# Performance work log

Measured on AMD Instinct MI355X. Metric: run time of the kernel, lower is better.

Reference implementation:

```python
import jax, jax.numpy as jnp
import numpy as np

B, S, E = 8, 4096, 2048
LATENT, HEAD = 64, 128


def setup_inputs() -> dict:
    key = jax.random.key(0)
    ks = jax.random.split(key, 5)
    sd = lambda n: 1.0 / np.sqrt(n)
    return {
        "x": jax.random.normal(ks[0], (B, S, E), dtype=jnp.float32),
        "w_dkv": jax.random.normal(ks[1], (E, LATENT), dtype=jnp.float32) * sd(E),
        "w_k": jax.random.normal(ks[2], (LATENT, HEAD), dtype=jnp.float32) * sd(LATENT),
        "w_v": jax.random.normal(ks[3], (LATENT, HEAD), dtype=jnp.float32) * sd(LATENT),
        "w_q": jax.random.normal(ks[4], (E, HEAD), dtype=jnp.float32) * sd(E),
    }


def reference(x, w_dkv, w_k, w_v, w_q):
    # x: [B,S,E]. kv_cache=None path: cache = fresh compressed latents.
    latent = jnp.einsum('bse,el->bsl', x, w_dkv)          # [B,S,latent] compressed KV cache
    k = jnp.einsum('bsl,lh->bsh', latent, w_k)            # decompress keys   [B,S,head]
    v = jnp.einsum('bsl,lh->bsh', latent, w_v)            # decompress values [B,S,head]
    q = jnp.einsum('bse,eh->bsh', x, w_q)                 # queries [B,S,head]
    scale = w_q.shape[-1] ** -0.5
    scores = jnp.einsum('bqh,bkh->bqk', q, k) * scale     # [B,S,S]
    seq = x.shape[1]
    causal = jnp.tril(jnp.ones((seq, seq), dtype=bool))   # tril(seq, cache_len)
    scores = jnp.where(causal, scores, -jnp.inf)
    attn = jax.nn.softmax(scores, axis=-1)                # dropout p=0 (eval)
    out = jnp.einsum('bqk,bkh->bqh', attn, v)             # [B,S,head]
    return out, latent
```

## Files before the change

### kernel.cpp

```cpp
#include <hip/hip_runtime.h>

typedef __bf16 bf16;
typedef __bf16 bf16x2 __attribute__((ext_vector_type(2)));
typedef __bf16 bf16x4 __attribute__((ext_vector_type(4)));
typedef __bf16 bf16x8 __attribute__((ext_vector_type(8)));
typedef float  f32x4  __attribute__((ext_vector_type(4)));

#define MFMA16(a,b,c) __builtin_amdgcn_mfma_f32_16x16x32_bf16((a),(b),(c),0,0,0)

constexpr int Bn = 8, Sn = 4096, En = 2048, Ln = 64, Hn = 128;
constexpr int Mrows = Bn * Sn;

__device__ __forceinline__ void load_lds_16(const bf16* g, bf16* l) {
    __builtin_amdgcn_global_load_lds(
        (const __attribute__((address_space(1))) uint32_t*)g,
        (__attribute__((address_space(3))) uint32_t*)l, 16, 0, 0);
}

__global__ __launch_bounds__(256) void transpose_cvt(const float* __restrict__ in,
                                                     bf16* __restrict__ out,
                                                     int K, int N) {
    int tid = blockIdx.x * 256 + threadIdx.x;
    if (tid >= K * N) return;
    int k = tid / N, n = tid - k * N;
    out[n * K + k] = (bf16)in[tid];
}

__global__ __launch_bounds__(512) void gemm_xw(const float* __restrict__ x,
                                               const bf16* __restrict__ wT,
                                               const bf16* __restrict__ wkT,
                                               const bf16* __restrict__ wvT,
                                               float* __restrict__ latent_out,
                                               bf16* __restrict__ q_out,
                                               bf16* __restrict__ k_out,
                                               bf16* __restrict__ vT_out) {
    __shared__ __align__(16) bf16 As[64 * 72];
    __shared__ __align__(16) bf16 Bs[192 * 64];
    const int lane = threadIdx.x & 63;
    const int wave = threadIdx.x >> 6;
    const int col  = lane & 15, quad = lane >> 4;
    const int mgrp  = wave >> 1;
    const int nhalf = wave & 1;
    const int mblock = blockIdx.x * 64;

    f32x4 acc[6];
#pragma unroll
    for (int t = 0; t < 6; ++t) acc[t] = (f32x4){0.f, 0.f, 0.f, 0.f};

    const int bsub = lane >> 3;
    const int bkg0 = lane & 7;
    const int akc  = threadIdx.x & 15;
    const int arow0 = threadIdx.x >> 4;

    for (int step = 0; step < 32; ++step) {
        __syncthreads();
#pragma unroll
        for (int j = 0; j < 3; ++j) {
            int nr0 = wave * 24 + j * 8;
            int n = nr0 + bsub;
            int kgrp = bkg0 ^ bsub;
            const bf16* g = wT + (size_t)n * En + step * 64 + kgrp * 8;
            load_lds_16(g, &Bs[nr0 * 64]);
        }
#pragma unroll
        for (int p = 0; p < 2; ++p) {
            int row = p * 32 + arow0;
            f32x4 v = *(const f32x4*)(x + (size_t)(mblock + row) * En + step * 64 + akc * 4);
            bf16x4 c;
#pragma unroll
            for (int j = 0; j < 4; ++j) c[j] = (bf16)v[j];
            *(bf16x4*)(&As[row * 72 + akc * 4]) = c;
        }
        __syncthreads();
#pragma unroll
        for (int ks2 = 0; ks2 < 2; ++ks2) {
            bf16x8 a = *(const bf16x8*)(&As[(mgrp * 16 + col) * 72 + ks2 * 32 + quad * 8]);
#pragma unroll
            for (int t = 0; t < 6; ++t) {
                int n = nhalf * 96 + t * 16 + col;
                int sg = (ks2 * 4 + quad) ^ (col & 7);
                bf16x8 b = *(const bf16x8*)(&Bs[n * 64 + sg * 8]);
                acc[t] = MFMA16(a, b, acc[t]);
            }
        }
    }
    __syncthreads();
    if (nhalf == 0) {
#pragma unroll
        for (int t = 0; t < 4; ++t)
#pragma unroll
            for (int r = 0; r < 4; ++r)
                As[(mgrp * 16 + quad * 4 + r) * 72 + t * 16 + col] = (bf16)acc[t][r];
    }
#pragma unroll
    for (int t = 0; t < 6; ++t) {
        int gnt = nhalf * 6 + t;
#pragma unroll
        for (int r = 0; r < 4; ++r) {
            int row = mblock + mgrp * 16 + quad * 4 + r;
            if (gnt < 4) latent_out[(size_t)row * Ln + gnt * 16 + col] = acc[t][r];
            else         q_out[(size_t)row * Hn + (gnt - 4) * 16 + col] = (bf16)acc[t][r];
        }
    }
    __syncthreads();
    const bf16* w2 = (nhalf == 0) ? wkT : wvT;
    f32x4 kv[8];
#pragma unroll
    for (int nt = 0; nt < 8; ++nt) kv[nt] = (f32x4){0.f, 0.f, 0.f, 0.f};
#pragma unroll
    for (int ks = 0; ks < 2; ++ks) {
        bf16x8 a = *(const bf16x8*)(&As[(mgrp * 16 + col) * 72 + ks * 32 + quad * 8]);
#pragma unroll
        for (int nt = 0; nt < 8; ++nt) {
            bf16x8 b = *(const bf16x8*)(w2 + (nt * 16 + col) * Ln + ks * 32 + quad * 8);
            kv[nt] = MFMA16(a, b, kv[nt]);
        }
    }
    if (nhalf == 0) {
#pragma unroll
        for (int nt = 0; nt < 8; ++nt)
#pragma unroll
            for (int r = 0; r < 4; ++r) {
                int row = mblock + mgrp * 16 + quad * 4 + r;
                k_out[(size_t)row * Hn + nt * 16 + col] = (bf16)kv[nt][r];
            }
    } else {
        int bb = mblock >> 12;
        int sbase = (mblock & 4095) + mgrp * 16 + quad * 4;
#pragma unroll
        for (int nt = 0; nt < 8; ++nt) {
            bf16x4 pv;
#pragma unroll
            for (int r = 0; r < 4; ++r) pv[r] = (bf16)kv[nt][r];
            *(bf16x4*)(vT_out + ((size_t)bb * Hn + nt * 16 + col) * Sn + sbase) = pv;
        }
    }
}

__global__ __launch_bounds__(256, 3) void mla_attn(const bf16* __restrict__ qg,
                                                   const bf16* __restrict__ kg,
                                                   const bf16* __restrict__ vtg,
                                                   float* __restrict__ outg) {
    __shared__ __align__(16) bf16 Ks[64 * 128];
    __shared__ __align__(16) bf16 VtS[128 * 64];
    __shared__ __align__(16) bf16 Pb[4][16][72];
    const int lane = threadIdx.x & 63;
    const int wave = threadIdx.x >> 6;
    const int col  = lane & 15, quad = lane >> 4;
    const int rank  = blockIdx.x;
    const int qtile = 63 - (rank >> 3);
    const int bb    = rank & 7;
    const int qbase = qtile * 64;
    const bf16* kb  = kg  + (size_t)bb * Sn * Hn;
    const bf16* vbT = vtg + (size_t)bb * Sn * Hn;

    bf16x8 qf[4];
    {
        const bf16* qrow = qg + ((size_t)bb * Sn + qbase + wave * 16 + col) * Hn;
#pragma unroll
        for (int ks = 0; ks < 4; ++ks)
            qf[ks] = *(const bf16x8*)(qrow + ks * 32 + quad * 8);
    }
    f32x4 o[8];
#pragma unroll
    for (int t = 0; t < 8; ++t) o[t] = (f32x4){0.f, 0.f, 0.f, 0.f};
    float m_run = -3.0e38f;
    float l_run = 0.f;
    const float scale = 0.08838834764831845f;
    const int qrow = wave * 16 + col;

    for (int kt = 0; kt <= qtile; ++kt) {
        __syncthreads();
#pragma unroll
        for (int ii = 0; ii < 4; ++ii) {
            int i = wave * 4 + ii;
            int key = 4 * i + (lane >> 4);
            int p = lane & 15;
            int g = (p & 8) | ((p & 7) ^ (key & 7));
            const bf16* src = kb + (size_t)(kt * 64 + key) * Hn + g * 8;
            load_lds_16(src, Ks + i * 512);
        }
#pragma unroll
        for (int ii = 0; ii < 4; ++ii) {
            int i = wave * 4 + ii;
            int r = i * 8 + (lane >> 3);
            int c = lane & 7;
            int cs = c ^ (r & 7);
            const bf16* src = vbT + (size_t)r * Sn + kt * 64 + cs * 8;
            load_lds_16(src, VtS + i * 512);
        }
        __syncthreads();

        f32x4 sa[4];
#pragma unroll
        for (int nt = 0; nt < 4; ++nt) {
            sa[nt] = (f32x4){0.f, 0.f, 0.f, 0.f};
#pragma unroll
            for (int ks = 0; ks < 4; ++ks) {
                int key = nt * 16 + col;
                int g = ks * 4 + quad;
                int pos = (g & 8) | ((g & 7) ^ (col & 7));
                bf16x8 kfr = *(const bf16x8*)(Ks + key * 128 + pos * 8);
                sa[nt] = MFMA16(kfr, qf[ks], sa[nt]);
            }
        }
        float p_[4][4];
        if (kt == qtile) {
#pragma unroll
            for (int nt = 0; nt < 4; ++nt)
#pragma unroll
                for (int r = 0; r < 4; ++r) {
                    float s = sa[nt][r] * scale;
                    if (nt * 16 + quad * 4 + r > qrow) s = -1.0e30f;
                    p_[nt][r] = s;
                }
        } else {
#pragma unroll
            for (int nt = 0; nt < 4; ++nt)
#pragma unroll
                for (int r = 0; r < 4; ++r) p_[nt][r] = sa[nt][r] * scale;
        }
        float mt = p_[0][0];
#pragma unroll
        for (int nt = 0; nt < 4; ++nt)
#pragma unroll
            for (int r = 0; r < 4; ++r) mt = fmaxf(mt, p_[nt][r]);
        mt = fmaxf(mt, __shfl_xor(mt, 16, 64));
        mt = fmaxf(mt, __shfl_xor(mt, 32, 64));
        float mn = fmaxf(m_run, mt);
        float alpha = __expf(m_run - mn);
        m_run = mn;
        float rs = 0.f;
#pragma unroll
        for (int nt = 0; nt < 4; ++nt)
#pragma unroll
            for (int r = 0; r < 4; ++r) {
                float p = __expf(p_[nt][r] - mn);
                p_[nt][r] = p;
                rs += p;
            }
        rs += __shfl_xor(rs, 16, 64);
        rs += __shfl_xor(rs, 32, 64);
        l_run = l_run * alpha + rs;
        float al[4];
#pragma unroll
        for (int r = 0; r < 4; ++r) al[r] = __shfl(alpha, quad * 4 + r, 64);
#pragma unroll
        for (int t = 0; t < 8; ++t)
#pragma unroll
            for (int r = 0; r < 4; ++r) o[t][r] *= al[r];
#pragma unroll
        for (int nt = 0; nt < 4; ++nt) {
            bf16x4 pv;
#pragma unroll
            for (int r = 0; r < 4; ++r) pv[r] = (bf16)p_[nt][r];
            *(bf16x4*)(&Pb[wave][col][((nt ^ (col >> 2)) & 3) * 16 + quad * 4]) = pv;
        }
#pragma unroll
        for (int ks = 0; ks < 2; ++ks) {
            int pos = (ks * 32 + quad * 8) ^ ((col >> 2) * 16);
            bf16x8 pa = *(const bf16x8*)(&Pb[wave][col][pos]);
#pragma unroll
            for (int nt = 0; nt < 8; ++nt) {
                int row = nt * 16 + col;
                int g = (ks * 4 + quad) ^ (row & 7);
                bf16x8 bv = *(const bf16x8*)(VtS + row * 64 + g * 8);
                o[nt] = MFMA16(pa, bv, o[nt]);
            }
        }
    }
    float lr[4];
#pragma unroll
    for (int r = 0; r < 4; ++r) lr[r] = __shfl(l_run, quad * 4 + r, 64);
#pragma unroll
    for (int r = 0; r < 4; ++r) {
        float inv = 1.0f / lr[r];
        int row = qbase + wave * 16 + quad * 4 + r;
        float* orow = outg + ((size_t)bb * Sn + row) * Hn;
#pragma unroll
        for (int t = 0; t < 8; ++t)
            orow[t * 16 + col] = o[t][r] * inv;
    }
}

extern "C" void kernel_launch(void* const* d_in, const int* in_sizes, int n_in,
                              void* d_out, int out_size, void* d_ws, size_t ws_size,
                              hipStream_t stream) {
    const float* x     = (const float*)d_in[0];
    const float* w_dkv = (const float*)d_in[1];
    const float* w_k   = (const float*)d_in[2];
    const float* w_v   = (const float*)d_in[3];
    const float* w_q   = (const float*)d_in[4];

    float* out        = (float*)d_out;
    float* latent_out = out + (size_t)Mrows * Hn;

    char* ws = (char*)d_ws;
    bf16* q_ws = (bf16*)(ws);
    bf16* k_ws = (bf16*)(ws + (size_t)8  * 1024 * 1024);
    bf16* v_ws = (bf16*)(ws + (size_t)16 * 1024 * 1024);
    bf16* wT   = (bf16*)(ws + (size_t)24 * 1024 * 1024);
    bf16* wkT  = (bf16*)(ws + (size_t)24 * 1024 * 1024 + 768 * 1024);
    bf16* wvT  = (bf16*)(ws + (size_t)24 * 1024 * 1024 + 784 * 1024);

    transpose_cvt<<<(En * Ln + 255) / 256, 256, 0, stream>>>(w_dkv, wT, En, Ln);
    transpose_cvt<<<(En * Hn + 255) / 256, 256, 0, stream>>>(w_q, wT + (size_t)64 * En, En, Hn);
    transpose_cvt<<<(Ln * Hn + 255) / 256, 256, 0, stream>>>(w_k, wkT, Ln, Hn);
    transpose_cvt<<<(Ln * Hn + 255) / 256, 256, 0, stream>>>(w_v, wvT, Ln, Hn);
    gemm_xw<<<Mrows / 64, 512, 0, stream>>>(x, wT, wkT, wvT, latent_out, q_ws, k_ws, v_ws);
    mla_attn<<<Sn / 64 * Bn, 256, 0, stream>>>(q_ws, k_ws, v_ws, out);
}
```

Baseline: 533.2 us.

## Double-buffer K/V tiles in LDS to overlap global loads with MFMA compute

Gives the attention kernel two LDS buffers for the K and V^T tiles. The next tile's async global-to-LDS loads are issued before computing on the current one, with a partial vmcnt wait and explicit barriers. The aim is to hide global load latency behind the QK and PV MFMA work. LDS use doubles, so launch bounds drop from 3 to 2 blocks per CU, which lowers occupancy and the latency hiding that comes from multiple resident blocks.

```diff
diff --git a/kernel.cpp b/kernel.cpp
--- a/kernel.cpp
+++ b/kernel.cpp
@@ -137,12 +137,12 @@
     }
 }
 
-__global__ __launch_bounds__(256, 3) void mla_attn(const bf16* __restrict__ qg,
+__global__ __launch_bounds__(256, 2) void mla_attn(const bf16* __restrict__ qg,
                                                    const bf16* __restrict__ kg,
                                                    const bf16* __restrict__ vtg,
                                                    float* __restrict__ outg) {
-    __shared__ __align__(16) bf16 Ks[64 * 128];
-    __shared__ __align__(16) bf16 VtS[128 * 64];
+    __shared__ __align__(16) bf16 Ks[2][64 * 128];
+    __shared__ __align__(16) bf16 VtS[2][128 * 64];
     __shared__ __align__(16) bf16 Pb[4][16][72];
     const int lane = threadIdx.x & 63;
     const int wave = threadIdx.x >> 6;
@@ -169,27 +169,37 @@
     const float scale = 0.08838834764831845f;
     const int qrow = wave * 16 + col;
 
-    for (int kt = 0; kt <= qtile; ++kt) {
-        __syncthreads();
+    auto stage = [&](int buf, int kt_) {
 #pragma unroll
         for (int ii = 0; ii < 4; ++ii) {
             int i = wave * 4 + ii;
             int key = 4 * i + (lane >> 4);
             int p = lane & 15;
             int g = (p & 8) | ((p & 7) ^ (key & 7));
-            const bf16* src = kb + (size_t)(kt * 64 + key) * Hn + g * 8;
-            load_lds_16(src, Ks + i * 512);
+            load_lds_16(kb + (size_t)(kt_ * 64 + key) * Hn + g * 8, &Ks[buf][i * 512]);
         }
 #pragma unroll
         for (int ii = 0; ii < 4; ++ii) {
             int i = wave * 4 + ii;
             int r = i * 8 + (lane >> 3);
-            int c = lane & 7;
-            int cs = c ^ (r & 7);
-            const bf16* src = vbT + (size_t)r * Sn + kt * 64 + cs * 8;
-            load_lds_16(src, VtS + i * 512);
-        }
-        __syncthreads();
+            int cs = (lane & 7) ^ (r & 7);
+            load_lds_16(vbT + (size_t)r * Sn + kt_ * 64 + cs * 8, &VtS[buf][i * 512]);
+        }
+    };
+
+    stage(0, 0);
+    for (int kt = 0; kt <= qtile; ++kt) {
+        const int cur = kt & 1;
+        if (kt < qtile) {
+            stage(cur ^ 1, kt + 1);
+            asm volatile("s_waitcnt vmcnt(8)" ::: "memory");
+        } else {
+            asm volatile("s_waitcnt vmcnt(0)" ::: "memory");
+        }
+        __builtin_amdgcn_s_barrier();
+        __builtin_amdgcn_sched_barrier(0);
+        const bf16* KsC = Ks[cur];
+        const bf16* VtC = VtS[cur];
 
         f32x4 sa[4];
 #pragma unroll
@@ -200,7 +210,7 @@
                 int key = nt * 16 + col;
                 int g = ks * 4 + quad;
                 int pos = (g & 8) | ((g & 7) ^ (col & 7));
-                bf16x8 kfr = *(const bf16x8*)(Ks + key * 128 + pos * 8);
+                bf16x8 kfr = *(const bf16x8*)(KsC + key * 128 + pos * 8);
                 sa[nt] = MFMA16(kfr, qf[ks], sa[nt]);
             }
         }
@@ -264,10 +274,12 @@
             for (int nt = 0; nt < 8; ++nt) {
                 int row = nt * 16 + col;
                 int g = (ks * 4 + quad) ^ (row & 7);
-                bf16x8 bv = *(const bf16x8*)(VtS + row * 64 + g * 8);
+                bf16x8 bv = *(const bf16x8*)(VtC + row * 64 + g * 8);
                 o[nt] = MFMA16(pa, bv, o[nt]);
             }
         }
+        __builtin_amdgcn_sched_barrier(0);
+        __builtin_amdgcn_s_barrier();
     }
     float lr[4];
 #pragma unroll
```

Result: faster. 510.7 us (-4.2%).
